# Kernel optimization log

Hardware: AMD Instinct MI355X
Metric: run time of the kernel (lower is better)

Reference implementation:

```python
import jax, jax.numpy as jnp
import numpy as np

N_NODES = 50000
MAX_DEG = 32
FEAT = 128


def setup_inputs() -> dict:
    key = jax.random.key(0)
    mailbox = jax.random.normal(key, (N_NODES, MAX_DEG, FEAT), dtype=jnp.float32)
    return {"mailbox": mailbox}


def reference(mailbox):
    # Aggregator.forward: c = aggre(node.mailbox['m'])
    # Canonical concrete aggre (MeanAggregator): mean over the neighbor axis.
    # mailbox: [N, deg, F] -> c: [N, F]
    c = jnp.mean(mailbox, axis=1)
    return c
```

## Files before the change

kernel.cpp:

```cpp
#include <hip/hip_runtime.h>


constexpr int N_NODES = 50000;
constexpr int MAX_DEG = 32;
constexpr int FEAT    = 128;
constexpr int F4      = FEAT / 4;
constexpr int TOTAL4  = N_NODES * F4;

__global__ __launch_bounds__(256) void mean_agg_kernel(
    const float4* __restrict__ in, float4* __restrict__ out) {
    int idx = blockIdx.x * blockDim.x + threadIdx.x;
    if (idx >= TOTAL4) return;
    int n = idx >> 5;
    int j = idx & (F4 - 1);
    const float4* p = in + (size_t)n * MAX_DEG * F4 + j;
    float4 acc = make_float4(0.f, 0.f, 0.f, 0.f);
#pragma unroll
    for (int d = 0; d < MAX_DEG; ++d) {
        float4 v = p[(size_t)d * F4];
        acc.x += v.x; acc.y += v.y; acc.z += v.z; acc.w += v.w;
    }
    const float s = 1.0f / MAX_DEG;
    acc.x *= s; acc.y *= s; acc.z *= s; acc.w *= s;
    out[idx] = acc;
}

extern "C" void kernel_launch(void* const* d_in, const int* in_sizes, int n_in,
                              void* d_out, int out_size, void* d_ws, size_t ws_size,
                              hipStream_t stream) {
    const float4* in = (const float4*)d_in[0];
    float4* out = (float4*)d_out;
    const int block = 256;
    const int grid = (TOTAL4 + block - 1) / block;
    mean_agg_kernel<<<grid, block, 0, stream>>>(in, out);
}
```

Measured before the change: 1.003 ms.

## Split degree reduction across thread groups with shared-memory partial sums

Each block now handles two nodes, and each node's 32 neighbor rows are split across four 32-thread groups. Each group sums 8 rows with two independent accumulators, then shared memory combines the four partials before scaling and writing. The aim is more in-flight loads and more blocks to hide memory latency in this bandwidth-bound reduction. In exchange it adds a __syncthreads and leaves most threads idle during the final reduction and store.

```diff
diff --git a/kernel.cpp b/kernel.cpp
--- a/kernel.cpp
+++ b/kernel.cpp
@@ -3,26 +3,49 @@
 
 constexpr int N_NODES = 50000;
 constexpr int MAX_DEG = 32;
-constexpr int FEAT    = 128;
-constexpr int F4      = FEAT / 4;
-constexpr int TOTAL4  = N_NODES * F4;
+constexpr int F4      = 32;
+constexpr int NODES_PER_BLOCK = 2;
 
-__global__ __launch_bounds__(256) void mean_agg_kernel(
+__global__ __launch_bounds__(256, 8) void mean_agg_kernel(
     const float4* __restrict__ in, float4* __restrict__ out) {
-    int idx = blockIdx.x * blockDim.x + threadIdx.x;
-    if (idx >= TOTAL4) return;
-    int n = idx >> 5;
-    int j = idx & (F4 - 1);
-    const float4* p = in + (size_t)n * MAX_DEG * F4 + j;
-    float4 acc = make_float4(0.f, 0.f, 0.f, 0.f);
+    __shared__ float4 part[256];
+
+    const int t  = threadIdx.x;
+    const int nb = blockIdx.x * NODES_PER_BLOCK;
+    const int ln = t >> 7;
+    const int l  = t & 127;
+    const int rq = l >> 5;
+    const int j  = l & 31;
+
+    const float4* p = in + ((size_t)(nb + ln) * MAX_DEG + rq * 8) * F4 + j;
+
+    float4 a = make_float4(0.f, 0.f, 0.f, 0.f);
+    float4 b = make_float4(0.f, 0.f, 0.f, 0.f);
 #pragma unroll
-    for (int d = 0; d < MAX_DEG; ++d) {
-        float4 v = p[(size_t)d * F4];
-        acc.x += v.x; acc.y += v.y; acc.z += v.z; acc.w += v.w;
+    for (int k = 0; k < 8; k += 2) {
+        float4 v0 = p[(size_t)k * F4];
+        float4 v1 = p[(size_t)(k + 1) * F4];
+        a.x += v0.x; a.y += v0.y; a.z += v0.z; a.w += v0.w;
+        b.x += v1.x; b.y += v1.y; b.z += v1.z; b.w += v1.w;
     }
-    const float s = 1.0f / MAX_DEG;
-    acc.x *= s; acc.y *= s; acc.z *= s; acc.w *= s;
-    out[idx] = acc;
+    a.x += b.x; a.y += b.y; a.z += b.z; a.w += b.w;
+    part[t] = a;
+    __syncthreads();
+
+    if (t < 64) {
+        const int base = (t >> 5) * 128 + (t & 31);
+        float4 s0 = part[base];
+        float4 s1 = part[base + 32];
+        float4 s2 = part[base + 64];
+        float4 s3 = part[base + 96];
+        float4 r;
+        const float s = 1.0f / MAX_DEG;
+        r.x = (s0.x + s1.x + s2.x + s3.x) * s;
+        r.y = (s0.y + s1.y + s2.y + s3.y) * s;
+        r.z = (s0.z + s1.z + s2.z + s3.z) * s;
+        r.w = (s0.w + s1.w + s2.w + s3.w) * s;
+        out[(size_t)nb * F4 + t] = r;
+    }
 }
 
 extern "C" void kernel_launch(void* const* d_in, const int* in_sizes, int n_in,
@@ -30,7 +53,6 @@
                               hipStream_t stream) {
     const float4* in = (const float4*)d_in[0];
     float4* out = (float4*)d_out;
-    const int block = 256;
-    const int grid = (TOTAL4 + block - 1) / block;
-    mean_agg_kernel<<<grid, block, 0, stream>>>(in, out);
+    const int grid = N_NODES / NODES_PER_BLOCK;
+    mean_agg_kernel<<<grid, 256, 0, stream>>>(in, out);
 }
```

After: 1.011 ms. About the same (+0.8%).
